# Optimization experiments

Hardware: AMD Instinct MI355X
Metric: run time of the kernel (lower is better)

The kernel has to match this reference:

```python
import jax, jax.numpy as jnp
import numpy as np

OMODE, PMODE, NZ = 2, 4, 8
NY = NX = 512
NPY = NPX = 128
NPOS = 1024
BATCH = 64


def setup_inputs() -> dict:
    key = jax.random.key(0)
    ks = jax.random.split(key, 8)
    obja = jax.random.uniform(ks[0], (OMODE, NZ, NY, NX), jnp.float32, 0.9, 1.0)
    objp = 0.1 * jax.random.normal(ks[1], (OMODE, NZ, NY, NX), jnp.float32)
    probe = jax.random.normal(ks[2], (PMODE, NPY, NPX, 2), jnp.float32)
    probe_pos_shifts = 0.5 * jax.random.normal(ks[3], (NPOS, 2), jnp.float32)
    theta = jax.random.normal(ks[4], (NPY, NPX), jnp.float32)
    H = jnp.stack([jnp.cos(theta), jnp.sin(theta)], axis=-1)  # unit-modulus Fresnel phasor (re, im)
    omode_occu = jax.nn.softmax(jax.random.normal(ks[5], (OMODE,), jnp.float32))
    indices = jax.random.randint(ks[6], (BATCH,), 0, NPOS, jnp.int32)
    crop_pos = jax.random.randint(ks[7], (NPOS, 2), 0, NY - NPY, jnp.int32)
    return {"obja": obja, "objp": objp, "probe": probe,
            "probe_pos_shifts": probe_pos_shifts, "H": H, "omode_occu": omode_occu,
            "indices": indices, "crop_pos": crop_pos}


def reference(obja, objp, probe, probe_pos_shifts, H, omode_occu, indices, crop_pos):
    npy, npx = probe.shape[1], probe.shape[2]
    probe_c = probe[..., 0] + 1j * probe[..., 1]   # (pmode, Npy, Npx) complex64
    H_c = H[..., 0] + 1j * H[..., 1]               # (Npy, Npx) complex64

    # --- indexed patch gather: (omode, nz, N, Npy, Npx) -> (N, omode, nz, Npy, Npx) ---
    cy = crop_pos[indices, 0]
    cx = crop_pos[indices, 1]
    gy = cy[:, None, None] + jnp.arange(npy, dtype=jnp.int32)[None, :, None]  # (N, Npy, 1)
    gx = cx[:, None, None] + jnp.arange(npx, dtype=jnp.int32)[None, None, :]  # (N, 1, Npx)
    pa = jnp.transpose(obja[:, :, gy, gx], (2, 0, 1, 3, 4))
    pp = jnp.transpose(objp[:, :, gy, gx], (2, 0, 1, 3, 4))
    T = pa * jnp.exp(1j * pp)  # transmission per slice, (N, omode, nz, Npy, Npx)

    # --- sub-pixel Fourier probe shifts (imshift_batch) ---
    kpy = jnp.fft.fftfreq(npy).astype(jnp.float32)
    kpx = jnp.fft.fftfreq(npx).astype(jnp.float32)
    sh = probe_pos_shifts[indices]  # (N, 2)
    ramp = jnp.exp(-2j * jnp.pi * (kpy[None, :, None] * sh[:, 0, None, None]
                                   + kpx[None, None, :] * sh[:, 1, None, None]))  # (N, Npy, Npx)
    probes = jnp.fft.ifft2(jnp.fft.fft2(probe_c)[None] * ramp[:, None])  # (N, pmode, Npy, Npx)

    # --- multislice propagation: psi (N, omode, pmode, Npy, Npx) ---
    psi = probes[:, None]
    nz = T.shape[2]
    for z in range(nz):
        psi = psi * T[:, :, z, None]
        if z < nz - 1:
            psi = jnp.fft.ifft2(jnp.fft.fft2(psi) * H_c)

    # --- far-field detector intensity, mode-incoherent sum ---
    dp = jnp.einsum('o,nopyx->nyx', omode_occu, jnp.abs(jnp.fft.fft2(psi)) ** 2)
    return dp
```

## Files before the change

### kernel.cpp

```cpp
#include <hip/hip_runtime.h>

static constexpr int OMODE = 2, PMODE = 4, NZ = 8;
static constexpr int NYX = 512;
static constexpr int NP  = 128;
static constexpr int BATCH = 64;
static constexpr int LSTR = 129;
static constexpr float INV_N2 = 1.0f / 16384.0f;

typedef float v2f __attribute__((ext_vector_type(2)));

__device__ __forceinline__ int br7(int x) { return (int)(__brev((unsigned)x) >> 25); }

__device__ __forceinline__ v2f splat2(float s) { return (v2f){s, s}; }
__device__ __forceinline__ v2f swapv(v2f v) { return __builtin_shufflevector(v, v, 1, 0); }
__device__ __forceinline__ v2f cmulv(v2f a, float br_, float bi_) {
  return a * splat2(br_) + swapv(a) * (v2f){-bi_, bi_};
}
__device__ __forceinline__ v2f cmulvv(v2f a, v2f b) {
  return a * splat2(b.x) + swapv(a) * (v2f){-b.y, b.y};
}

template<int CTRL>
__device__ __forceinline__ float dppf(float x) {
  int i = __float_as_int(x);
  int r = __builtin_amdgcn_update_dpp(i, i, CTRL, 0xF, 0xF, false);
  return __int_as_float(r);
}
template<int CTRL>
__device__ __forceinline__ v2f dpp2(v2f v) {
  return (v2f){dppf<CTRL>(v.x), dppf<CTRL>(v.y)};
}
template<int OFS>
__device__ __forceinline__ v2f swz2(v2f v) {
  v2f t;
  t.x = __int_as_float(__builtin_amdgcn_ds_swizzle(__float_as_int(v.x), OFS));
  t.y = __int_as_float(__builtin_amdgcn_ds_swizzle(__float_as_int(v.y), OFS));
  return t;
}
__device__ __forceinline__ v2f bp2(v2f v, int bp32) {
  v2f t;
  t.x = __int_as_float(__builtin_amdgcn_ds_bpermute(bp32, __float_as_int(v.x)));
  t.y = __int_as_float(__builtin_amdgcn_ds_bpermute(bp32, __float_as_int(v.y)));
  return t;
}

struct Tw {
  float tc6, ts6;
  float g[6];
  float dwr[6], dwi[6];
};

template<int S> __device__ __forceinline__ v2f twd(v2f d, const Tw& tw) {
  return d * splat2(tw.dwr[S]) + swapv(d) * (v2f){-tw.dwi[S], tw.dwi[S]};
}
template<int S> __device__ __forceinline__ v2f twc(v2f a, const Tw& tw) {
  return a * splat2(tw.dwr[S]) + swapv(a) * (v2f){tw.dwi[S], -tw.dwi[S]};
}

#define DIF_SWZ_STAGE8(OFS, S)                                             \
  {                                                                        \
    v2f tA[8], tB[8];                                                      \
    _Pragma("unroll") for (int k = 0; k < 8; ++k) {                        \
      tA[k] = swz2<OFS>(A[k]);                                            \
      tB[k] = swz2<OFS>(B[k]);                                            \
    }                                                                      \
    _Pragma("unroll") for (int k = 0; k < 8; ++k) {                        \
      A[k] = twd<S>(tA[k] + splat2(tw.g[S]) * A[k], tw);                   \
      B[k] = twd<S>(tB[k] + splat2(tw.g[S]) * B[k], tw);                   \
    }                                                                      \
  }

#define DIT_SWZ_STAGE8(OFS, S)                                             \
  {                                                                        \
    v2f mA[8], mB[8], tA[8], tB[8];                                        \
    _Pragma("unroll") for (int k = 0; k < 8; ++k) {                        \
      mA[k] = twc<S>(A[k], tw);                                           \
      mB[k] = twc<S>(B[k], tw);                                           \
    }                                                                      \
    _Pragma("unroll") for (int k = 0; k < 8; ++k) {                        \
      tA[k] = swz2<OFS>(mA[k]);                                           \
      tB[k] = swz2<OFS>(mB[k]);                                           \
    }                                                                      \
    _Pragma("unroll") for (int k = 0; k < 8; ++k) {                        \
      A[k] = tA[k] + splat2(tw.g[S]) * mA[k];                              \
      B[k] = tB[k] + splat2(tw.g[S]) * mB[k];                              \
    }                                                                      \
  }

__device__ __forceinline__ void dif128_x8(v2f A[8], v2f B[8], const Tw& tw, int bp32) {
#pragma unroll
  for (int k = 0; k < 8; ++k) {
    v2f d = A[k] - B[k];
    A[k] = A[k] + B[k];
    B[k] = d * splat2(tw.tc6) + swapv(d) * (v2f){tw.ts6, -tw.ts6};
  }
  {
    v2f tA[8], tB[8];
#pragma unroll
    for (int k = 0; k < 8; ++k) { tA[k] = bp2(A[k], bp32); tB[k] = bp2(B[k], bp32); }
#pragma unroll
    for (int k = 0; k < 8; ++k) {
      A[k] = twd<5>(tA[k] + splat2(tw.g[5]) * A[k], tw);
      B[k] = twd<5>(tB[k] + splat2(tw.g[5]) * B[k], tw);
    }
  }
  DIF_SWZ_STAGE8(0x401F, 4)
  DIF_SWZ_STAGE8(0x201F, 3)
  DIF_SWZ_STAGE8(0x101F, 2)
#pragma unroll
  for (int k = 0; k < 8; ++k) {
    A[k] = twd<1>(dpp2<0x4E>(A[k]) + splat2(tw.g[1]) * A[k], tw);
    B[k] = twd<1>(dpp2<0x4E>(B[k]) + splat2(tw.g[1]) * B[k], tw);
    A[k] = dpp2<0xB1>(A[k]) + splat2(tw.g[0]) * A[k];
    B[k] = dpp2<0xB1>(B[k]) + splat2(tw.g[0]) * B[k];
  }
}

__device__ __forceinline__ void dit128_x8(v2f A[8], v2f B[8], const Tw& tw, int bp32) {
#pragma unroll
  for (int k = 0; k < 8; ++k) {
    A[k] = dpp2<0xB1>(A[k]) + splat2(tw.g[0]) * A[k];
    B[k] = dpp2<0xB1>(B[k]) + splat2(tw.g[0]) * B[k];
    v2f mA = twc<1>(A[k], tw), mB = twc<1>(B[k], tw);
    A[k] = dpp2<0x4E>(mA) + splat2(tw.g[1]) * mA;
    B[k] = dpp2<0x4E>(mB) + splat2(tw.g[1]) * mB;
  }
  DIT_SWZ_STAGE8(0x101F, 2)
  DIT_SWZ_STAGE8(0x201F, 3)
  DIT_SWZ_STAGE8(0x401F, 4)
  {
    v2f mA[8], mB[8], tA[8], tB[8];
#pragma unroll
    for (int k = 0; k < 8; ++k) { mA[k] = twc<5>(A[k], tw); mB[k] = twc<5>(B[k], tw); }
#pragma unroll
    for (int k = 0; k < 8; ++k) { tA[k] = bp2(mA[k], bp32); tB[k] = bp2(mB[k], bp32); }
#pragma unroll
    for (int k = 0; k < 8; ++k) {
      A[k] = tA[k] + splat2(tw.g[5]) * mA[k];
      B[k] = tB[k] + splat2(tw.g[5]) * mB[k];
    }
  }
#pragma unroll
  for (int k = 0; k < 8; ++k) {
    v2f m = B[k] * splat2(tw.tc6) + swapv(B[k]) * (v2f){-tw.ts6, tw.ts6};
    B[k] = A[k] - m;
    A[k] = A[k] + m;
  }
}

__device__ __forceinline__ void init_tw(Tw& tw, int lane) {
  tw.g[0] = (lane & 1) ? -1.f : 1.f;
#pragma unroll
  for (int s = 1; s < 6; ++s) {
    int h = 1 << s;
    int j = lane & (h - 1);
    float ang = 3.14159265358979f * (float)j / (float)h;
    float ts_, tc_;
    __sincosf(ang, &ts_, &tc_);
    bool up = (lane >> s) & 1;
    tw.g[s]   = up ? -1.f : 1.f;
    tw.dwr[s] = up ? tc_ : 1.f;
    tw.dwi[s] = up ? -ts_ : 0.f;
  }
  __sincosf(3.14159265358979f * (float)lane * (1.f / 64.f), &tw.ts6, &tw.tc6);
}

__global__ void __launch_bounds__(256) init_hpre(const float* __restrict__ H,
                                                 float2* __restrict__ hp) {
  int i = blockIdx.x * blockDim.x + threadIdx.x;
  if (i >= NP * NP) return;
  int px = i >> 7, py = i & (NP - 1);
  int ky = br7(py), kx = br7(px);
  hp[px * NP + py] = make_float2(H[(ky * NP + kx) * 2 + 0] * INV_N2,
                                 H[(ky * NP + kx) * 2 + 1] * INV_N2);
}

__global__ void __launch_bounds__(256) init_ramp(const float* __restrict__ shifts,
                                                 const int* __restrict__ indices,
                                                 float2* __restrict__ rampy,
                                                 float2* __restrict__ rampx) {
  int i = blockIdx.x * blockDim.x + threadIdx.x;
  if (i >= 2 * BATCH * NP) return;
  int which = (i >= BATCH * NP) ? 1 : 0;
  int r = i - which * BATCH * NP;
  int n = r >> 7, slot = r & (NP - 1);
  int pos = indices[n];
  float sh = shifts[2 * pos + which];
  int k = br7(slot);
  float f = (float)(k < 64 ? k : k - 128) * (1.f / 128.f);
  float s, c;
  __sincosf(-6.28318530717959f * f * sh, &s, &c);
  if (!which) rampy[n * NP + slot] = make_float2(c * INV_N2, s * INV_N2);
  else        rampx[n * NP + slot] = make_float2(c, s);
}

__global__ void __launch_bounds__(256) init_T(const float* __restrict__ obja,
                                              const float* __restrict__ objp,
                                              float2* __restrict__ T) {
  int i = blockIdx.x * 256 + threadIdx.x;
  if (i >= OMODE * NZ * NYX * NYX) return;
  float a = obja[i], ph = objp[i];
  float s, c;
  __sincosf(ph, &s, &c);
  T[i] = make_float2(a * c, a * s);
}

__global__ void __launch_bounds__(256) reduce_dp(const float* __restrict__ part,
                                                 const float* __restrict__ occu,
                                                 float* __restrict__ dp) {
  int i = blockIdx.x * 256 + threadIdx.x;
  if (i >= BATCH * NP * NP) return;
  int n = i >> 14;
  int r = i & (NP * NP - 1);
  int ky = r >> 7, kx = r & (NP - 1);
  const float* b = part + ((size_t)n * 8 << 14) + (kx << 7) + ky;
  float w0 = occu[0], w1 = occu[1];
  float s = 0.f;
#pragma unroll
  for (int j = 0; j < 8; ++j) s = fmaf(b[(size_t)j << 14], (j < 4 ? w0 : w1), s);
  dp[i] = s;
}

__global__ void
__attribute__((amdgpu_flat_work_group_size(512, 512), amdgpu_waves_per_eu(2, 2)))
shift_probe(const float* __restrict__ probe,
            const float2* __restrict__ rampy, const float2* __restrict__ rampx,
            float2* __restrict__ ps)
{
  extern __shared__ v2f fld[];
  const int blk  = blockIdx.x;
  const int n    = blk >> 2;
  const int p    = blk & 3;
  const int tid  = threadIdx.x;
  const int wid  = tid >> 6;
  const int lane = tid & 63;
  const int bp32 = (lane ^ 32) << 2;

  Tw tw;
  init_tw(tw, lane);

  const v2f* probe2 = (const v2f*)probe;
#pragma unroll 1
  for (int k0 = 0; k0 < 16; k0 += 8) {
    int r0 = wid * 16 + k0;
    v2f A[8], B[8];
#pragma unroll
    for (int kk = 0; kk < 8; ++kk) {
      A[kk] = probe2[(p * NP + r0 + kk) * NP + lane];
      B[kk] = probe2[(p * NP + r0 + kk) * NP + lane + 64];
    }
    dif128_x8(A, B, tw, bp32);
#pragma unroll
    for (int kk = 0; kk < 8; ++kk) {
      fld[(r0 + kk) * LSTR + lane]      = A[kk];
      fld[(r0 + kk) * LSTR + lane + 64] = B[kk];
    }
  }
  __syncthreads();

  {
    float2 t0 = rampy[n * NP + lane];
    float2 t1 = rampy[n * NP + lane + 64];
    v2f ry0 = (v2f){t0.x, t0.y}, ry1 = (v2f){t1.x, t1.y};
#pragma unroll 1
    for (int k0 = 0; k0 < 16; k0 += 8) {
      int c0 = wid * 16 + k0;
      float2 rx[8];
#pragma unroll
      for (int kk = 0; kk < 8; ++kk) rx[kk] = rampx[n * NP + c0 + kk];
      v2f A[8], B[8];
#pragma unroll
      for (int kk = 0; kk < 8; ++kk) {
        A[kk] = fld[lane * LSTR + c0 + kk];
        B[kk] = fld[(lane + 64) * LSTR + c0 + kk];
      }
      dif128_x8(A, B, tw, bp32);
#pragma unroll
      for (int kk = 0; kk < 8; ++kk) {
        v2f m;
        m = cmulv(ry0, rx[kk].x, rx[kk].y); A[kk] = cmulvv(A[kk], m);
        m = cmulv(ry1, rx[kk].x, rx[kk].y); B[kk] = cmulvv(B[kk], m);
      }
      dit128_x8(A, B, tw, bp32);
#pragma unroll
      for (int kk = 0; kk < 8; ++kk) {
        fld[lane * LSTR + c0 + kk]        = A[kk];
        fld[(lane + 64) * LSTR + c0 + kk] = B[kk];
      }
    }
    __syncthreads();
  }

  float2* out = ps + ((size_t)blk << 14);
#pragma unroll 1
  for (int k0 = 0; k0 < 16; k0 += 8) {
    int r0 = wid * 16 + k0;
    v2f A[8], B[8];
#pragma unroll
    for (int kk = 0; kk < 8; ++kk) {
      A[kk] = fld[(r0 + kk) * LSTR + lane];
      B[kk] = fld[(r0 + kk) * LSTR + lane + 64];
    }
    dit128_x8(A, B, tw, bp32);
#pragma unroll
    for (int kk = 0; kk < 8; ++kk) {
      out[(r0 + kk) * NP + lane]      = make_float2(A[kk].x, A[kk].y);
      out[(r0 + kk) * NP + lane + 64] = make_float2(B[kk].x, B[kk].y);
    }
  }
}

__global__ void
__attribute__((amdgpu_flat_work_group_size(512, 512), amdgpu_waves_per_eu(2, 2)))
ptycho_chain(
    const float* __restrict__ obja, const float* __restrict__ objp,
    const float* __restrict__ probe, const float* __restrict__ shifts,
    const float* __restrict__ H, const float2* __restrict__ hpre,
    const float2* __restrict__ rampy, const float2* __restrict__ rampx,
    const float2* __restrict__ Tpre, const float2* __restrict__ Ps,
    const float* __restrict__ occu, const int* __restrict__ indices,
    const int* __restrict__ crop, float* __restrict__ dp,
    float* __restrict__ part, int mode_ws, int mode_T, int mode_ps)
{
  extern __shared__ v2f fld[];

  const int blk  = blockIdx.x;
  const int n    = blk >> 3;
  const int o    = (blk >> 2) & 1;
  const int p    = blk & 3;
  const int tid  = threadIdx.x;
  const int wid  = tid >> 6;
  const int lane = tid & 63;
  const int bp32 = (lane ^ 32) << 2;

  const int   pos = indices[n];
  const int   cy  = crop[2 * pos + 0];
  const int   cx  = crop[2 * pos + 1];
  const float wocc = occu[o];

  Tw tw;
  init_tw(tw, lane);

  auto ramp_mul_fb = [&](v2f& A, v2f& B, int c) {
    float sh0v = shifts[2 * pos], sh1v = shifts[2 * pos + 1];
    int kxc = br7(c);
    float fx = (float)(kxc < 64 ? kxc : kxc - 128) * (1.f / 128.f);
    int ky0 = br7(lane);
    float fy0 = (float)(ky0 < 64 ? ky0 : ky0 - 128) * (1.f / 128.f);
    int ky1 = ky0 + 1;
    float fy1 = (float)(ky1 < 64 ? ky1 : ky1 - 128) * (1.f / 128.f);
    float com = fx * sh1v;
    float s0, c0_, s1, c1_;
    __sincosf(-6.28318530717959f * (fy0 * sh0v + com), &s0, &c0_);
    __sincosf(-6.28318530717959f * (fy1 * sh0v + com), &s1, &c1_);
    A = cmulv(A, c0_ * INV_N2, s0 * INV_N2);
    B = cmulv(B, c1_ * INV_N2, s1 * INV_N2);
  };
  auto h_mul_fb = [&](v2f& A, v2f& B, int c) {
    int kx = br7(c), ky0 = br7(lane);
    float hr0 = H[(ky0 * NP + kx) * 2], hi0 = H[(ky0 * NP + kx) * 2 + 1];
    float hr1 = H[((ky0 + 1) * NP + kx) * 2], hi1 = H[((ky0 + 1) * NP + kx) * 2 + 1];
    A = cmulv(A, hr0 * INV_N2, hi0 * INV_N2);
    B = cmulv(B, hr1 * INV_N2, hi1 * INV_N2);
  };

  auto cphase = [&](int mode) {
    v2f ry0, ry1;
    if (mode == 0 && mode_ws) {
      float2 t0 = rampy[n * NP + lane];
      float2 t1 = rampy[n * NP + lane + 64];
      ry0 = (v2f){t0.x, t0.y}; ry1 = (v2f){t1.x, t1.y};
    }
#pragma unroll 1
    for (int k0 = 0; k0 < 16; k0 += 8) {
      int c0 = wid * 16 + k0;
      float2 h0[8], h1[8], rx[8];
      if (mode == 1 && mode_ws) {
#pragma unroll
        for (int kk = 0; kk < 8; ++kk) {
          h0[kk] = hpre[(c0 + kk) * NP + lane];
          h1[kk] = hpre[(c0 + kk) * NP + lane + 64];
        }
      }
      if (mode == 0 && mode_ws) {
#pragma unroll
        for (int kk = 0; kk < 8; ++kk) rx[kk] = rampx[n * NP + c0 + kk];
      }
      v2f A[8], B[8];
#pragma unroll
      for (int kk = 0; kk < 8; ++kk) {
        A[kk] = fld[lane * LSTR + c0 + kk];
        B[kk] = fld[(lane + 64) * LSTR + c0 + kk];
      }
      dif128_x8(A, B, tw, bp32);
      if (mode == 0) {
        if (mode_ws) {
#pragma unroll
          for (int kk = 0; kk < 8; ++kk) {
            v2f m;
            m = cmulv(ry0, rx[kk].x, rx[kk].y); A[kk] = cmulvv(A[kk], m);
            m = cmulv(ry1, rx[kk].x, rx[kk].y); B[kk] = cmulvv(B[kk], m);
          }
        } else {
#pragma unroll
          for (int kk = 0; kk < 8; ++kk) ramp_mul_fb(A[kk], B[kk], c0 + kk);
        }
      } else {
        if (mode_ws) {
#pragma unroll
          for (int kk = 0; kk < 8; ++kk) {
            A[kk] = cmulv(A[kk], h0[kk].x, h0[kk].y);
            B[kk] = cmulv(B[kk], h1[kk].x, h1[kk].y);
          }
        } else {
#pragma unroll
          for (int kk = 0; kk < 8; ++kk) h_mul_fb(A[kk], B[kk], c0 + kk);
        }
      }
      dit128_x8(A, B, tw, bp32);
#pragma unroll
      for (int kk = 0; kk < 8; ++kk) {
        fld[lane * LSTR + c0 + kk]        = A[kk];
        fld[(lane + 64) * LSTR + c0 + kk] = B[kk];
      }
    }
    __syncthreads();
  };

  auto rphase = [&](int z) {
#pragma unroll 1
    for (int k0 = 0; k0 < 16; k0 += 8) {
      int r0 = wid * 16 + k0;
      size_t ob = ((size_t)(o * NZ + z) * NYX + (size_t)(cy + r0)) * NYX + cx;
      v2f A[8], B[8];
#pragma unroll
      for (int kk = 0; kk < 8; ++kk) {
        A[kk] = fld[(r0 + kk) * LSTR + lane];
        B[kk] = fld[(r0 + kk) * LSTR + lane + 64];
      }
      if (mode_T) {
        float2 t0[8], t1[8];
#pragma unroll
        for (int kk = 0; kk < 8; ++kk) {
          t0[kk] = Tpre[ob + (size_t)kk * NYX + lane];
          t1[kk] = Tpre[ob + (size_t)kk * NYX + lane + 64];
        }
        dit128_x8(A, B, tw, bp32);
#pragma unroll
        for (int kk = 0; kk < 8; ++kk) {
          A[kk] = cmulv(A[kk], t0[kk].x, t0[kk].y);
          B[kk] = cmulv(B[kk], t1[kk].x, t1[kk].y);
        }
      } else {
        float pa0[8], ph0[8], pa1[8], ph1[8];
#pragma unroll
        for (int kk = 0; kk < 8; ++kk) {
          pa0[kk] = obja[ob + (size_t)kk * NYX + lane];
          ph0[kk] = objp[ob + (size_t)kk * NYX + lane];
          pa1[kk] = obja[ob + (size_t)kk * NYX + lane + 64];
          ph1[kk] = objp[ob + (size_t)kk * NYX + lane + 64];
        }
        dit128_x8(A, B, tw, bp32);
#pragma unroll
        for (int kk = 0; kk < 8; ++kk) {
          float s, c;
          __sincosf(ph0[kk], &s, &c); A[kk] = cmulv(A[kk], pa0[kk] * c, pa0[kk] * s);
          __sincosf(ph1[kk], &s, &c); B[kk] = cmulv(B[kk], pa1[kk] * c, pa1[kk] * s);
        }
      }
      dif128_x8(A, B, tw, bp32);
#pragma unroll
      for (int kk = 0; kk < 8; ++kk) {
        fld[(r0 + kk) * LSTR + lane]      = A[kk];
        fld[(r0 + kk) * LSTR + lane + 64] = B[kk];
      }
    }
    __syncthreads();
  };

  if (mode_ps) {
    const float2* psf = Ps + ((size_t)((n << 2) + p) << 14);
#pragma unroll 1
    for (int k0 = 0; k0 < 16; k0 += 8) {
      int r0 = wid * 16 + k0;
      size_t ob = ((size_t)(o * NZ + 0) * NYX + (size_t)(cy + r0)) * NYX + cx;
      v2f A[8], B[8];
#pragma unroll
      for (int kk = 0; kk < 8; ++kk) {
        float2 p0 = psf[(r0 + kk) * NP + lane];
        float2 p1 = psf[(r0 + kk) * NP + lane + 64];
        float2 t0 = Tpre[ob + (size_t)kk * NYX + lane];
        float2 t1 = Tpre[ob + (size_t)kk * NYX + lane + 64];
        A[kk] = cmulv((v2f){p0.x, p0.y}, t0.x, t0.y);
        B[kk] = cmulv((v2f){p1.x, p1.y}, t1.x, t1.y);
      }
      dif128_x8(A, B, tw, bp32);
#pragma unroll
      for (int kk = 0; kk < 8; ++kk) {
        fld[(r0 + kk) * LSTR + lane]      = A[kk];
        fld[(r0 + kk) * LSTR + lane + 64] = B[kk];
      }
    }
    __syncthreads();
  } else {
    const v2f* probe2 = (const v2f*)probe;
#pragma unroll 1
    for (int k0 = 0; k0 < 16; k0 += 8) {
      int r0 = wid * 16 + k0;
      v2f A[8], B[8];
#pragma unroll
      for (int kk = 0; kk < 8; ++kk) {
        A[kk] = probe2[(p * NP + r0 + kk) * NP + lane];
        B[kk] = probe2[(p * NP + r0 + kk) * NP + lane + 64];
      }
      dif128_x8(A, B, tw, bp32);
#pragma unroll
      for (int kk = 0; kk < 8; ++kk) {
        fld[(r0 + kk) * LSTR + lane]      = A[kk];
        fld[(r0 + kk) * LSTR + lane + 64] = B[kk];
      }
    }
    __syncthreads();
    cphase(0);
    rphase(0);
  }

#pragma unroll 1
  for (int z = 1; z < NZ; ++z) {
    cphase(1);
    rphase(z);
  }

#pragma unroll 1
  for (int k0 = 0; k0 < 16; k0 += 8) {
    int c0 = wid * 16 + k0;
    v2f A[8], B[8];
#pragma unroll
    for (int kk = 0; kk < 8; ++kk) {
      A[kk] = fld[lane * LSTR + c0 + kk];
      B[kk] = fld[(lane + 64) * LSTR + c0 + kk];
    }
    dif128_x8(A, B, tw, bp32);
    int ky0 = br7(lane);
#pragma unroll
    for (int kk = 0; kk < 8; ++kk) {
      float m0 = fmaf(A[kk].x, A[kk].x, A[kk].y * A[kk].y);
      float m1 = fmaf(B[kk].x, B[kk].x, B[kk].y * B[kk].y);
      if (mode_ws) {
        size_t b0 = ((size_t)blk << 14) + (size_t)br7(c0 + kk) * NP;
        part[b0 + ky0]     = m0;
        part[b0 + ky0 + 1] = m1;
      } else {
        size_t base = ((size_t)n << 14);
        atomicAdd(&dp[base + (size_t)ky0 * NP + br7(c0 + kk)],       m0 * wocc);
        atomicAdd(&dp[base + (size_t)(ky0 + 1) * NP + br7(c0 + kk)], m1 * wocc);
      }
    }
  }
}

extern "C" void kernel_launch(void* const* d_in, const int* in_sizes, int n_in,
                              void* d_out, int out_size, void* d_ws, size_t ws_size,
                              hipStream_t stream) {
  const float* obja   = (const float*)d_in[0];
  const float* objp   = (const float*)d_in[1];
  const float* probe  = (const float*)d_in[2];
  const float* shifts = (const float*)d_in[3];
  const float* H      = (const float*)d_in[4];
  const float* occu   = (const float*)d_in[5];
  const int*   indices = (const int*)d_in[6];
  const int*   crop    = (const int*)d_in[7];
  float* dp = (float*)d_out;

  const size_t part_bytes  = (size_t)BATCH * OMODE * PMODE * NP * NP * sizeof(float);
  const size_t hpre_bytes  = (size_t)NP * NP * sizeof(float2);
  const size_t ramp_bytes  = (size_t)BATCH * NP * sizeof(float2);
  const size_t T_bytes     = (size_t)OMODE * NZ * NYX * NYX * sizeof(float2);
  const size_t ps_bytes    = (size_t)BATCH * PMODE * NP * NP * sizeof(float2);
  const size_t need_ws = part_bytes + hpre_bytes + 2 * ramp_bytes;
  const size_t need_T  = need_ws + T_bytes;
  const size_t need_ps = need_T + ps_bytes;

  int mode_ws = (ws_size >= need_ws) ? 1 : 0;
  int mode_T  = (ws_size >= need_T) ? 1 : 0;
  int mode_ps = (ws_size >= need_ps) ? 1 : 0;
  float*  part  = (float*)d_ws;
  float2* hpre  = (float2*)((char*)d_ws + part_bytes);
  float2* rampy = (float2*)((char*)d_ws + part_bytes + hpre_bytes);
  float2* rampx = (float2*)((char*)d_ws + part_bytes + hpre_bytes + ramp_bytes);
  float2* Tpre  = (float2*)((char*)d_ws + need_ws);
  float2* Ps    = (float2*)((char*)d_ws + need_T);

  if (mode_ws) {
    hipLaunchKernelGGL(init_hpre, dim3((NP * NP + 255) / 256), dim3(256), 0,
                       stream, H, hpre);
    hipLaunchKernelGGL(init_ramp, dim3((2 * BATCH * NP + 255) / 256), dim3(256), 0,
                       stream, shifts, indices, rampy, rampx);
  } else {
    hipMemsetAsync(d_out, 0, (size_t)out_size * sizeof(float), stream);
  }
  if (mode_T) {
    hipLaunchKernelGGL(init_T, dim3((OMODE * NZ * NYX * NYX + 255) / 256), dim3(256),
                       0, stream, obja, objp, Tpre);
  }

  const int lds_bytes = NP * LSTR * (int)sizeof(float2);
  if (mode_ps) {
    hipFuncSetAttribute((const void*)shift_probe,
                        hipFuncAttributeMaxDynamicSharedMemorySize, lds_bytes);
    hipLaunchKernelGGL(shift_probe, dim3(BATCH * PMODE), dim3(512),
                       lds_bytes, stream, probe, rampy, rampx, Ps);
  }

  hipFuncSetAttribute((const void*)ptycho_chain,
                      hipFuncAttributeMaxDynamicSharedMemorySize, lds_bytes);
  hipLaunchKernelGGL(ptycho_chain, dim3(BATCH * OMODE * PMODE), dim3(512),
                     lds_bytes, stream,
                     obja, objp, probe, shifts, H, hpre, rampy, rampx, Tpre, Ps,
                     occu, indices, crop, dp, part, mode_ws, mode_T, mode_ps);
  if (mode_ws) {
    hipLaunchKernelGGL(reduce_dp, dim3((BATCH * NP * NP + 255) / 256), dim3(256),
                       0, stream, part, occu, dp);
  }
}
```

Before: 415.5 us.

## Replace radix-2 cross-lane FFT stages with fused radix-4 stage pairs

The in-wavefront 128-point FFTs now merge stages 5/4 and 3/2 into radix-4 butterflies. Each lane fetches three partners (swizzle or bpermute) and combines them with precomputed per-lane coefficients. This removes the intermediate twiddle multiplies and register shuffles between stage pairs, lowering the ALU instruction count. In exchange, each pair needs three cross-lane exchanges instead of two, the twiddle state per lane grows, and register pressure rises.

New measurement: 518.5 us. 1.25x slower.

```diff
diff --git a/kernel.cpp b/kernel.cpp
--- a/kernel.cpp
+++ b/kernel.cpp
@@ -19,6 +19,9 @@
 __device__ __forceinline__ v2f cmulvv(v2f a, v2f b) {
   return a * splat2(b.x) + swapv(a) * (v2f){-b.y, b.y};
 }
+__device__ __forceinline__ v2f cpk(float cx, float cy, v2f v, v2f acc) {
+  return acc + splat2(cx) * v + (v2f){-cy, cy} * swapv(v);
+}
 
 template<int CTRL>
 __device__ __forceinline__ float dppf(float x) {
@@ -37,132 +40,162 @@
   t.y = __int_as_float(__builtin_amdgcn_ds_swizzle(__float_as_int(v.y), OFS));
   return t;
 }
-__device__ __forceinline__ v2f bp2(v2f v, int bp32) {
+__device__ __forceinline__ v2f bp2(v2f v, int idx) {
   v2f t;
-  t.x = __int_as_float(__builtin_amdgcn_ds_bpermute(bp32, __float_as_int(v.x)));
-  t.y = __int_as_float(__builtin_amdgcn_ds_bpermute(bp32, __float_as_int(v.y)));
+  t.x = __int_as_float(__builtin_amdgcn_ds_bpermute(idx, __float_as_int(v.x)));
+  t.y = __int_as_float(__builtin_amdgcn_ds_bpermute(idx, __float_as_int(v.y)));
   return t;
 }
 
 struct Tw {
   float tc6, ts6;
-  float g[6];
-  float dwr[6], dwi[6];
+  float g0;
+  float g1, dw1r, dw1i;
+  float gA54, A54x, A54y, B54x, B54y;
+  float gA32, A32x, A32y, B32x, B32y;
+  float ca23x, ca23y, c123x, c123y, c223x, c223y, c323x, c323y;
+  float ca45x, ca45y, c145x, c145y, c245x, c245y, c345x, c345y;
 };
 
-template<int S> __device__ __forceinline__ v2f twd(v2f d, const Tw& tw) {
-  return d * splat2(tw.dwr[S]) + swapv(d) * (v2f){-tw.dwi[S], tw.dwi[S]};
-}
-template<int S> __device__ __forceinline__ v2f twc(v2f a, const Tw& tw) {
-  return a * splat2(tw.dwr[S]) + swapv(a) * (v2f){tw.dwi[S], -tw.dwi[S]};
-}
-
-#define DIF_SWZ_STAGE8(OFS, S)                                             \
-  {                                                                        \
-    v2f tA[8], tB[8];                                                      \
-    _Pragma("unroll") for (int k = 0; k < 8; ++k) {                        \
-      tA[k] = swz2<OFS>(A[k]);                                            \
-      tB[k] = swz2<OFS>(B[k]);                                            \
-    }                                                                      \
-    _Pragma("unroll") for (int k = 0; k < 8; ++k) {                        \
-      A[k] = twd<S>(tA[k] + splat2(tw.g[S]) * A[k], tw);                   \
-      B[k] = twd<S>(tB[k] + splat2(tw.g[S]) * B[k], tw);                   \
-    }                                                                      \
-  }
-
-#define DIT_SWZ_STAGE8(OFS, S)                                             \
-  {                                                                        \
-    v2f mA[8], mB[8], tA[8], tB[8];                                        \
-    _Pragma("unroll") for (int k = 0; k < 8; ++k) {                        \
-      mA[k] = twc<S>(A[k], tw);                                           \
-      mB[k] = twc<S>(B[k], tw);                                           \
-    }                                                                      \
-    _Pragma("unroll") for (int k = 0; k < 8; ++k) {                        \
-      tA[k] = swz2<OFS>(mA[k]);                                           \
-      tB[k] = swz2<OFS>(mB[k]);                                           \
-    }                                                                      \
-    _Pragma("unroll") for (int k = 0; k < 8; ++k) {                        \
-      A[k] = tA[k] + splat2(tw.g[S]) * mA[k];                              \
-      B[k] = tB[k] + splat2(tw.g[S]) * mB[k];                              \
-    }                                                                      \
-  }
-
-__device__ __forceinline__ void dif128_x8(v2f A[8], v2f B[8], const Tw& tw, int bp32) {
+__device__ __forceinline__ void dif_coef(int j, int b0, int b1, float invH2,
+    float& gA, float& Ax, float& Ay, float& Bx, float& By) {
+  float th = 3.14159265358979f * (float)j * invH2;
+  float s1, c1, s2, c2, s3, c3;
+  __sincosf(th, &s1, &c1);
+  __sincosf(2.f * th, &s2, &c2);
+  __sincosf(3.f * th, &s3, &c3);
+  gA = b1 ? -1.f : 1.f;
+  if (!b1) {
+    if (!b0) { Ax = 1.f;  Ay = 0.f;  Bx = 1.f;  By = 0.f; }
+    else     { Ax = -c2;  Ay = s2;   Bx = c2;   By = -s2; }
+  } else {
+    if (!b0) { Ax = c1;   Ay = -s1;  Bx = -s1;  By = -c1; }
+    else     { Ax = s3;   Ay = c3;   Bx = c3;   By = -s3; }
+  }
+}
+__device__ __forceinline__ void dit_coef(int j, int b0, int b1, float invH2,
+    float& cax, float& cay, float& c1x, float& c1y,
+    float& c2x, float& c2y, float& c3x, float& c3y) {
+  float th = 3.14159265358979f * (float)j * invH2;
+  float s1, c1, s2, c2, s3, c3;
+  __sincosf(th, &s1, &c1);
+  __sincosf(2.f * th, &s2, &c2);
+  __sincosf(3.f * th, &s3, &c3);
+  if (!b1) {
+    if (!b0) { cax=1.f;  cay=0.f;  c1x=c2;  c1y=s2;  c2x=c1;  c2y=s1;  c3x=c3;  c3y=s3; }
+    else     { cax=-c2;  cay=-s2;  c1x=1.f; c1y=0.f; c2x=s3;  c2y=-c3; c3x=-s1; c3y=c1; }
+  } else {
+    if (!b0) { cax=-c1;  cay=-s1;  c1x=-c3; c1y=-s3; c2x=1.f; c2y=0.f; c3x=c2;  c3y=s2; }
+    else     { cax=-s3;  cay=c3;   c1x=s1;  c1y=-c1; c2x=-c2; c2y=-s2; c3x=1.f; c3y=0.f; }
+  }
+}
+
+__device__ __forceinline__ void init_tw(Tw& tw, int lane) {
+  tw.g0 = (lane & 1) ? -1.f : 1.f;
+  {
+    int j = lane & 1; bool up = (lane >> 1) & 1;
+    float s, c;
+    __sincosf(1.5707963268f * (float)j, &s, &c);
+    tw.g1   = up ? -1.f : 1.f;
+    tw.dw1r = up ? c : 1.f;
+    tw.dw1i = up ? -s : 0.f;
+  }
+  __sincosf(3.14159265358979f * (float)lane * (1.f / 64.f), &tw.ts6, &tw.tc6);
+  dif_coef(lane & 15, (lane >> 4) & 1, (lane >> 5) & 1, 1.f / 32.f,
+           tw.gA54, tw.A54x, tw.A54y, tw.B54x, tw.B54y);
+  dif_coef(lane & 3, (lane >> 2) & 1, (lane >> 3) & 1, 1.f / 8.f,
+           tw.gA32, tw.A32x, tw.A32y, tw.B32x, tw.B32y);
+  dit_coef(lane & 3, (lane >> 2) & 1, (lane >> 3) & 1, 1.f / 8.f,
+           tw.ca23x, tw.ca23y, tw.c123x, tw.c123y, tw.c223x, tw.c223y, tw.c323x, tw.c323y);
+  dit_coef(lane & 15, (lane >> 4) & 1, (lane >> 5) & 1, 1.f / 32.f,
+           tw.ca45x, tw.ca45y, tw.c145x, tw.c145y, tw.c245x, tw.c245y, tw.c345x, tw.c345y);
+}
+
+#define DIF_R4_PAIR(X, EX1, EX2, EX3, GA, AX, AY, BX, BY)                   \
+  {                                                                         \
+    v2f p1[8], p2[8], p3[8];                                                \
+    _Pragma("unroll") for (int k = 0; k < 8; ++k) p1[k] = EX1(X[k]);        \
+    _Pragma("unroll") for (int k = 0; k < 8; ++k) p2[k] = EX2(X[k]);        \
+    _Pragma("unroll") for (int k = 0; k < 8; ++k) p3[k] = EX3(X[k]);        \
+    _Pragma("unroll") for (int k = 0; k < 8; ++k) {                         \
+      v2f U = p2[k] + splat2(GA) * X[k];                                    \
+      v2f V = p3[k] + splat2(GA) * p1[k];                                   \
+      v2f z = splat2(AX) * U + (v2f){-(AY), (AY)} * swapv(U);               \
+      X[k] = cpk(BX, BY, V, z);                                             \
+    }                                                                       \
+  }
+
+#define DIT_R4_PAIR(X, EX1, EX2, EX3, CAX, CAY, C1X, C1Y, C2X, C2Y, C3X, C3Y) \
+  {                                                                         \
+    v2f p1[8], p2[8], p3[8];                                                \
+    _Pragma("unroll") for (int k = 0; k < 8; ++k) p1[k] = EX1(X[k]);        \
+    _Pragma("unroll") for (int k = 0; k < 8; ++k) p2[k] = EX2(X[k]);        \
+    _Pragma("unroll") for (int k = 0; k < 8; ++k) p3[k] = EX3(X[k]);        \
+    _Pragma("unroll") for (int k = 0; k < 8; ++k) {                         \
+      v2f z = splat2(CAX) * X[k] + (v2f){-(CAY), (CAY)} * swapv(X[k]);      \
+      z = cpk(C1X, C1Y, p1[k], z);                                          \
+      z = cpk(C2X, C2Y, p2[k], z);                                          \
+      X[k] = cpk(C3X, C3Y, p3[k], z);                                       \
+    }                                                                       \
+  }
+
+#define EX_SWZ4(v)  swz2<0x101F>(v)
+#define EX_SWZ8(v)  swz2<0x201F>(v)
+#define EX_SWZ12(v) swz2<0x301F>(v)
+#define EX_SWZ16(v) swz2<0x401F>(v)
+#define EX_BP32(v)  bp2(v, bp32)
+#define EX_BP48(v)  bp2(v, bp48)
+
+__device__ __forceinline__ void dif128_x8(v2f A[8], v2f B[8], const Tw& tw,
+                                          int bp32, int bp48) {
 #pragma unroll
   for (int k = 0; k < 8; ++k) {
     v2f d = A[k] - B[k];
     A[k] = A[k] + B[k];
     B[k] = d * splat2(tw.tc6) + swapv(d) * (v2f){tw.ts6, -tw.ts6};
   }
-  {
-    v2f tA[8], tB[8];
-#pragma unroll
-    for (int k = 0; k < 8; ++k) { tA[k] = bp2(A[k], bp32); tB[k] = bp2(B[k], bp32); }
-#pragma unroll
-    for (int k = 0; k < 8; ++k) {
-      A[k] = twd<5>(tA[k] + splat2(tw.g[5]) * A[k], tw);
-      B[k] = twd<5>(tB[k] + splat2(tw.g[5]) * B[k], tw);
-    }
-  }
-  DIF_SWZ_STAGE8(0x401F, 4)
-  DIF_SWZ_STAGE8(0x201F, 3)
-  DIF_SWZ_STAGE8(0x101F, 2)
+  DIF_R4_PAIR(A, EX_SWZ16, EX_BP32, EX_BP48, tw.gA54, tw.A54x, tw.A54y, tw.B54x, tw.B54y)
+  DIF_R4_PAIR(B, EX_SWZ16, EX_BP32, EX_BP48, tw.gA54, tw.A54x, tw.A54y, tw.B54x, tw.B54y)
+  DIF_R4_PAIR(A, EX_SWZ4, EX_SWZ8, EX_SWZ12, tw.gA32, tw.A32x, tw.A32y, tw.B32x, tw.B32y)
+  DIF_R4_PAIR(B, EX_SWZ4, EX_SWZ8, EX_SWZ12, tw.gA32, tw.A32x, tw.A32y, tw.B32x, tw.B32y)
 #pragma unroll
   for (int k = 0; k < 8; ++k) {
-    A[k] = twd<1>(dpp2<0x4E>(A[k]) + splat2(tw.g[1]) * A[k], tw);
-    B[k] = twd<1>(dpp2<0x4E>(B[k]) + splat2(tw.g[1]) * B[k], tw);
-    A[k] = dpp2<0xB1>(A[k]) + splat2(tw.g[0]) * A[k];
-    B[k] = dpp2<0xB1>(B[k]) + splat2(tw.g[0]) * B[k];
-  }
-}
-
-__device__ __forceinline__ void dit128_x8(v2f A[8], v2f B[8], const Tw& tw, int bp32) {
+    v2f d;
+    d = dpp2<0x4E>(A[k]) + splat2(tw.g1) * A[k];
+    A[k] = d * splat2(tw.dw1r) + swapv(d) * (v2f){-tw.dw1i, tw.dw1i};
+    d = dpp2<0x4E>(B[k]) + splat2(tw.g1) * B[k];
+    B[k] = d * splat2(tw.dw1r) + swapv(d) * (v2f){-tw.dw1i, tw.dw1i};
+    A[k] = dpp2<0xB1>(A[k]) + splat2(tw.g0) * A[k];
+    B[k] = dpp2<0xB1>(B[k]) + splat2(tw.g0) * B[k];
+  }
+}
+
+__device__ __forceinline__ void dit128_x8(v2f A[8], v2f B[8], const Tw& tw,
+                                          int bp32, int bp48) {
 #pragma unroll
   for (int k = 0; k < 8; ++k) {
-    A[k] = dpp2<0xB1>(A[k]) + splat2(tw.g[0]) * A[k];
-    B[k] = dpp2<0xB1>(B[k]) + splat2(tw.g[0]) * B[k];
-    v2f mA = twc<1>(A[k], tw), mB = twc<1>(B[k], tw);
-    A[k] = dpp2<0x4E>(mA) + splat2(tw.g[1]) * mA;
-    B[k] = dpp2<0x4E>(mB) + splat2(tw.g[1]) * mB;
-  }
-  DIT_SWZ_STAGE8(0x101F, 2)
-  DIT_SWZ_STAGE8(0x201F, 3)
-  DIT_SWZ_STAGE8(0x401F, 4)
-  {
-    v2f mA[8], mB[8], tA[8], tB[8];
-#pragma unroll
-    for (int k = 0; k < 8; ++k) { mA[k] = twc<5>(A[k], tw); mB[k] = twc<5>(B[k], tw); }
-#pragma unroll
-    for (int k = 0; k < 8; ++k) { tA[k] = bp2(mA[k], bp32); tB[k] = bp2(mB[k], bp32); }
-#pragma unroll
-    for (int k = 0; k < 8; ++k) {
-      A[k] = tA[k] + splat2(tw.g[5]) * mA[k];
-      B[k] = tB[k] + splat2(tw.g[5]) * mB[k];
-    }
-  }
+    A[k] = dpp2<0xB1>(A[k]) + splat2(tw.g0) * A[k];
+    B[k] = dpp2<0xB1>(B[k]) + splat2(tw.g0) * B[k];
+    v2f m;
+    m = A[k] * splat2(tw.dw1r) + swapv(A[k]) * (v2f){tw.dw1i, -tw.dw1i};
+    A[k] = dpp2<0x4E>(m) + splat2(tw.g1) * m;
+    m = B[k] * splat2(tw.dw1r) + swapv(B[k]) * (v2f){tw.dw1i, -tw.dw1i};
+    B[k] = dpp2<0x4E>(m) + splat2(tw.g1) * m;
+  }
+  DIT_R4_PAIR(A, EX_SWZ4, EX_SWZ8, EX_SWZ12, tw.ca23x, tw.ca23y, tw.c123x, tw.c123y,
+              tw.c223x, tw.c223y, tw.c323x, tw.c323y)
+  DIT_R4_PAIR(B, EX_SWZ4, EX_SWZ8, EX_SWZ12, tw.ca23x, tw.ca23y, tw.c123x, tw.c123y,
+              tw.c223x, tw.c223y, tw.c323x, tw.c323y)
+  DIT_R4_PAIR(A, EX_SWZ16, EX_BP32, EX_BP48, tw.ca45x, tw.ca45y, tw.c145x, tw.c145y,
+              tw.c245x, tw.c245y, tw.c345x, tw.c345y)
+  DIT_R4_PAIR(B, EX_SWZ16, EX_BP32, EX_BP48, tw.ca45x, tw.ca45y, tw.c145x, tw.c145y,
+              tw.c245x, tw.c245y, tw.c345x, tw.c345y)
 #pragma unroll
   for (int k = 0; k < 8; ++k) {
     v2f m = B[k] * splat2(tw.tc6) + swapv(B[k]) * (v2f){-tw.ts6, tw.ts6};
     B[k] = A[k] - m;
     A[k] = A[k] + m;
   }
-}
-
-__device__ __forceinline__ void init_tw(Tw& tw, int lane) {
-  tw.g[0] = (lane & 1) ? -1.f : 1.f;
-#pragma unroll
-  for (int s = 1; s < 6; ++s) {
-    int h = 1 << s;
-    int j = lane & (h - 1);
-    float ang = 3.14159265358979f * (float)j / (float)h;
-    float ts_, tc_;
-    __sincosf(ang, &ts_, &tc_);
-    bool up = (lane >> s) & 1;
-    tw.g[s]   = up ? -1.f : 1.f;
-    tw.dwr[s] = up ? tc_ : 1.f;
-    tw.dwi[s] = up ? -ts_ : 0.f;
-  }
-  __sincosf(3.14159265358979f * (float)lane * (1.f / 64.f), &tw.ts6, &tw.tc6);
 }
 
 __global__ void __launch_bounds__(256) init_hpre(const float* __restrict__ H,
@@ -235,6 +268,7 @@
   const int wid  = tid >> 6;
   const int lane = tid & 63;
   const int bp32 = (lane ^ 32) << 2;
+  const int bp48 = (lane ^ 48) << 2;
 
   Tw tw;
   init_tw(tw, lane);
@@ -249,7 +283,7 @@
       A[kk] = probe2[(p * NP + r0 + kk) * NP + lane];
       B[kk] = probe2[(p * NP + r0 + kk) * NP + lane + 64];
     }
-    dif128_x8(A, B, tw, bp32);
+    dif128_x8(A, B, tw, bp32, bp48);
 #pragma unroll
     for (int kk = 0; kk < 8; ++kk) {
       fld[(r0 + kk) * LSTR + lane]      = A[kk];
@@ -274,14 +308,14 @@
         A[kk] = fld[lane * LSTR + c0 + kk];
         B[kk] = fld[(lane + 64) * LSTR + c0 + kk];
       }
-      dif128_x8(A, B, tw, bp32);
+      dif128_x8(A, B, tw, bp32, bp48);
 #pragma unroll
       for (int kk = 0; kk < 8; ++kk) {
         v2f m;
         m = cmulv(ry0, rx[kk].x, rx[kk].y); A[kk] = cmulvv(A[kk], m);
         m = cmulv(ry1, rx[kk].x, rx[kk].y); B[kk] = cmulvv(B[kk], m);
       }
-      dit128_x8(A, B, tw, bp32);
+      dit128_x8(A, B, tw, bp32, bp48);
 #pragma unroll
       for (int kk = 0; kk < 8; ++kk) {
         fld[lane * LSTR + c0 + kk]        = A[kk];
@@ -301,7 +335,7 @@
       A[kk] = fld[(r0 + kk) * LSTR + lane];
       B[kk] = fld[(r0 + kk) * LSTR + lane + 64];
     }
-    dit128_x8(A, B, tw, bp32);
+    dit128_x8(A, B, tw, bp32, bp48);
 #pragma unroll
     for (int kk = 0; kk < 8; ++kk) {
       out[(r0 + kk) * NP + lane]      = make_float2(A[kk].x, A[kk].y);
@@ -332,6 +366,7 @@
   const int wid  = tid >> 6;
   const int lane = tid & 63;
   const int bp32 = (lane ^ 32) << 2;
+  const int bp48 = (lane ^ 48) << 2;
 
   const int   pos = indices[n];
   const int   cy  = crop[2 * pos + 0];
@@ -392,7 +427,7 @@
         A[kk] = fld[lane * LSTR + c0 + kk];
         B[kk] = fld[(lane + 64) * LSTR + c0 + kk];
       }
-      dif128_x8(A, B, tw, bp32);
+      dif128_x8(A, B, tw, bp32, bp48);
       if (mode == 0) {
         if (mode_ws) {
 #pragma unroll
@@ -417,7 +452,7 @@
           for (int kk = 0; kk < 8; ++kk) h_mul_fb(A[kk], B[kk], c0 + kk);
         }
       }
-      dit128_x8(A, B, tw, bp32);
+      dit128_x8(A, B, tw, bp32, bp48);
 #pragma unroll
       for (int kk = 0; kk < 8; ++kk) {
         fld[lane * LSTR + c0 + kk]        = A[kk];
@@ -445,7 +480,7 @@
           t0[kk] = Tpre[ob + (size_t)kk * NYX + lane];
           t1[kk] = Tpre[ob + (size_t)kk * NYX + lane + 64];
         }
-        dit128_x8(A, B, tw, bp32);
+        dit128_x8(A, B, tw, bp32, bp48);
 #pragma unroll
         for (int kk = 0; kk < 8; ++kk) {
           A[kk] = cmulv(A[kk], t0[kk].x, t0[kk].y);
@@ -460,7 +495,7 @@
           pa1[kk] = obja[ob + (size_t)kk * NYX + lane + 64];
           ph1[kk] = objp[ob + (size_t)kk * NYX + lane + 64];
         }
-        dit128_x8(A, B, tw, bp32);
+        dit128_x8(A, B, tw, bp32, bp48);
 #pragma unroll
         for (int kk = 0; kk < 8; ++kk) {
           float s, c;
@@ -468,7 +503,7 @@
           __sincosf(ph1[kk], &s, &c); B[kk] = cmulv(B[kk], pa1[kk] * c, pa1[kk] * s);
         }
       }
-      dif128_x8(A, B, tw, bp32);
+      dif128_x8(A, B, tw, bp32, bp48);
 #pragma unroll
       for (int kk = 0; kk < 8; ++kk) {
         fld[(r0 + kk) * LSTR + lane]      = A[kk];
@@ -494,7 +529,7 @@
         A[kk] = cmulv((v2f){p0.x, p0.y}, t0.x, t0.y);
         B[kk] = cmulv((v2f){p1.x, p1.y}, t1.x, t1.y);
       }
-      dif128_x8(A, B, tw, bp32);
+      dif128_x8(A, B, tw, bp32, bp48);
 #pragma unroll
       for (int kk = 0; kk < 8; ++kk) {
         fld[(r0 + kk) * LSTR + lane]      = A[kk];
@@ -513,7 +548,7 @@
         A[kk] = probe2[(p * NP + r0 + kk) * NP + lane];
         B[kk] = probe2[(p * NP + r0 + kk) * NP + lane + 64];
       }
-      dif128_x8(A, B, tw, bp32);
+      dif128_x8(A, B, tw, bp32, bp48);
 #pragma unroll
       for (int kk = 0; kk < 8; ++kk) {
         fld[(r0 + kk) * LSTR + lane]      = A[kk];
@@ -540,7 +575,7 @@
       A[kk] = fld[lane * LSTR + c0 + kk];
       B[kk] = fld[(lane + 64) * LSTR + c0 + kk];
     }
-    dif128_x8(A, B, tw, bp32);
+    dif128_x8(A, B, tw, bp32, bp48);
     int ky0 = br7(lane);
 #pragma unroll
     for (int kk = 0; kk < 8; ++kk) {
```
